# Performance work log

Measured on AMD Instinct MI355X. Metric: run time of the kernel, lower is better.

Reference implementation:

```python
import jax, jax.numpy as jnp
import numpy as np

C = 256  # channels
SHAPES = [(8, C, 80, 80), (8, C, 40, 40), (8, C, 20, 20), (8, C, 10, 10)]
EPS = 1e-8  # torch cosine_similarity eps


def _nearest_resize(x, H, W):
    # Matches F.interpolate(mode='nearest'): src_idx = floor(dst_idx * in/out)
    b, c, h, w = x.shape
    rows = (jnp.arange(H) * h) // H
    cols = (jnp.arange(W) * w) // W
    return x[:, :, rows[:, None], cols[None, :]]


def setup_inputs() -> dict:
    key = jax.random.key(0)
    ks = jax.random.split(key, 12)
    d = {}
    for i, s in enumerate(SHAPES):
        d[f"f{i}"] = jax.random.normal(ks[i], s, dtype=jnp.float32)
        d[f"w{i}"] = jax.random.normal(ks[4 + i], (C, C), dtype=jnp.float32) / jnp.sqrt(jnp.float32(C))
        d[f"b{i}"] = jax.random.normal(ks[8 + i], (C,), dtype=jnp.float32) * 0.01
    return d


def reference(f0, f1, f2, f3, w0, w1, w2, w3, b0, b1, b2, b3):
    feats = [f0, f1, f2, f3]
    ws = [w0, w1, w2, w3]
    bs = [b0, b1, b2, b3]
    H = max(f.shape[2] for f in feats)
    W = max(f.shape[3] for f in feats)
    proj = []
    for f, w, b in zip(feats, ws, bs):
        # 1x1 conv == per-pixel GEMM over channels
        p = jnp.einsum('bchw,oc->bohw', f, w) + b[None, :, None, None]
        if p.shape[2] != H or p.shape[3] != W:
            p = _nearest_resize(p, H, W)
        proj.append(p)
    B = proj[0].shape[0]
    N = len(proj)
    x = jnp.stack(proj, axis=1).reshape(B, N, C, H * W)  # [B,N,C,L]
    # Pairwise cosine similarity along channel dim at each spatial location,
    # then mean over locations (vectorized form of the O(N^2) torch loop).
    dot = jnp.einsum('bicl,bjcl->bijl', x, x)            # [B,N,N,L]
    nrm = jnp.sqrt(jnp.einsum('bicl,bicl->bil', x, x))   # [B,N,L]
    denom = jnp.maximum(nrm[:, :, None, :] * nrm[:, None, :, :], EPS)
    attn = (dot / denom).mean(axis=-1)                   # [B,N,N]
    return jax.nn.softmax(attn, axis=-1)
```

## Files before the change

kernel.cpp:

```cpp
#include <hip/hip_runtime.h>


#define CCH 256
#define WPITCH 40
#define SPITCH 264

typedef __attribute__((ext_vector_type(8))) short short8;
typedef __attribute__((ext_vector_type(4))) short short4_;
typedef __attribute__((ext_vector_type(4))) float float4_;

__device__ inline short f2bf(float x) {
    union { float f; unsigned u; } c; c.f = x;
    unsigned u = c.u + 0x7FFFu + ((c.u >> 16) & 1u);
    return (short)(u >> 16);
}
__device__ inline float bf2f(short b) {
    union { unsigned u; float f; } c; c.u = ((unsigned)(unsigned short)b) << 16;
    return c.f;
}

__device__ inline void dma16(const void* g, void* l) {
    __builtin_amdgcn_global_load_lds(
        (const __attribute__((address_space(1))) void*)g,
        (__attribute__((address_space(3))) void*)l, 16, 0, 0);
}

__global__ __launch_bounds__(256) void proj_small(
    const float* __restrict__ f1, const float* __restrict__ f2,
    const float* __restrict__ f3,
    const float* __restrict__ w0, const float* __restrict__ w1,
    const float* __restrict__ w2, const float* __restrict__ w3,
    const float* __restrict__ b1, const float* __restrict__ b2,
    const float* __restrict__ b3,
    short* __restrict__ u1, short* __restrict__ u2, short* __restrict__ u3,
    short* __restrict__ wp)
{
    __shared__ __align__(16) short Wt[256 * WPITCH];
    __shared__ __align__(16) short Ft[64 * WPITCH];

    const int blk = blockIdx.x;
    const int t = threadIdx.x;

    if (blk >= 272) {
        int id = (blk - 272) * 256 + t;
        int ks = id >> 10;
        int rest = id & 1023;
        int mt = rest >> 6;
        int fl = rest & 63;
        int ln = fl & 15, qd = fl >> 4;
        const float* src = w0 + (size_t)(mt * 16 + ln) * CCH + ks * 32 + qd * 8;
        short8 v;
#pragma unroll
        for (int j = 0; j < 8; ++j) v[j] = f2bf(src[j]);
        *(short8*)(wp + (size_t)id * 8) = v;
        return;
    }

    int b, tile, L;
    const float* F; const float* Wg; const float* bias; short* U;
    if (blk < 200)      { int r = blk;       b = r / 25; tile = r % 25; L = 1600; F = f1; Wg = w1; bias = b1; U = u1; }
    else if (blk < 256) { int r = blk - 200; b = r / 7;  tile = r % 7;  L = 400;  F = f2; Wg = w2; bias = b2; U = u2; }
    else                { int r = blk - 256; b = r / 2;  tile = r % 2;  L = 100;  F = f3; Wg = w3; bias = b3; U = u3; }

    const int lane = t & 63;
    const int wav  = t >> 6;
    const int ln   = lane & 15;
    const int quad = lane >> 4;
    const int pixbase = tile * 64;
    const float* Fb = F + (size_t)b * CCH * L;

    const int wo = t >> 2;
    const int wk = (t & 3) * 8;
    const int fpix = t & 63;
    const int fchunk = t >> 6;
    const int gpix0 = pixbase + fpix;
    const bool pin = gpix0 < L;
    const int gl0 = pin ? gpix0 : 0;

    float4_ wbufA[4], wbufB[4];
    float fbuf[8];
    auto loadW = [&](int ks) {
#pragma unroll
        for (int p = 0; p < 4; ++p) {
            const float* srcp = Wg + (size_t)(p * 64 + wo) * CCH + ks * 32 + wk;
            wbufA[p] = *(const float4_*)srcp;
            wbufB[p] = *(const float4_*)(srcp + 4);
        }
    };
    auto loadF = [&](int ks) {
        const float* fs = Fb + (size_t)(ks * 32 + fchunk * 8) * L + gl0;
#pragma unroll
        for (int j = 0; j < 8; ++j) fbuf[j] = fs[(size_t)j * L];
    };

    float4_ acc[16];
#pragma unroll
    for (int i = 0; i < 16; ++i) acc[i] = (float4_){0.f, 0.f, 0.f, 0.f};

    loadW(0); loadF(0);
    for (int ks = 0; ks < 8; ++ks) {
        __syncthreads();
#pragma unroll
        for (int p = 0; p < 4; ++p) {
            short8 v;
#pragma unroll
            for (int e = 0; e < 4; ++e) { v[e] = f2bf(wbufA[p][e]); v[e + 4] = f2bf(wbufB[p][e]); }
            *(short8*)(&Wt[(p * 64 + wo) * WPITCH + wk]) = v;
        }
        {
            short8 v;
#pragma unroll
            for (int j = 0; j < 8; ++j) v[j] = pin ? f2bf(fbuf[j]) : (short)0;
            *(short8*)(&Ft[fpix * WPITCH + fchunk * 8]) = v;
        }
        __syncthreads();
        const int ksn = (ks + 1) & 7;
        loadW(ksn); loadF(ksn);

        short8 bfrag = *(const short8*)(&Ft[(wav * 16 + ln) * WPITCH + quad * 8]);
#pragma unroll
        for (int mt = 0; mt < 16; ++mt) {
            short8 afrag = *(const short8*)(&Wt[(mt * 16 + ln) * WPITCH + quad * 8]);
            acc[mt] = __builtin_amdgcn_mfma_f32_16x16x32_bf16(afrag, bfrag, acc[mt], 0, 0, 0);
        }
    }

    float ss = 0.f;
#pragma unroll
    for (int mt = 0; mt < 16; ++mt) {
        float4_ bv = *(const float4_*)(bias + mt * 16 + quad * 4);
#pragma unroll
        for (int r = 0; r < 4; ++r) { float v = acc[mt][r] + bv[r]; acc[mt][r] = v; ss += v * v; }
    }
    ss += __shfl_xor(ss, 16);
    ss += __shfl_xor(ss, 32);
    const float inv = 1.f / sqrtf(fmaxf(ss, 1e-24f));

    const int gpixw = pixbase + wav * 16 + ln;
    if (gpixw < L) {
        short* dst = U + ((size_t)b * L + gpixw) * CCH;
#pragma unroll
        for (int mt = 0; mt < 16; ++mt) {
            short4_ v;
#pragma unroll
            for (int r = 0; r < 4; ++r) v[r] = f2bf(acc[mt][r] * inv);
            *(short4_*)(dst + mt * 16 + quad * 4) = v;
        }
    }
}

__global__ __launch_bounds__(256) void proj0_dots(
    const float* __restrict__ F, const short* __restrict__ wp,
    const float* __restrict__ bias,
    const short* __restrict__ u1, const short* __restrict__ u2,
    const short* __restrict__ u3,
    float* __restrict__ partial)
{
    __shared__ __align__(16) char smem[65536];
    short* Wb0 = (short*)smem;
    short* Wb1 = (short*)(smem + 16384);
    float* Fb0 = (float*)(smem + 32768);
    float* Fb1 = (float*)(smem + 49152);
    short* S1 = (short*)smem;
    short* S2 = (short*)(smem + 16896);
    short* S3 = (short*)(smem + 21120);
    float* redF = (float*)(smem + 22176);
    float* redC = (float*)(smem + 22224);

    const int c  = blockIdx.x;
    const int b  = blockIdx.y;
    const int R  = c / 5, C = c - R * 5;
    const int t  = threadIdx.x;
    const int lane = t & 63;
    const int wav  = t >> 6;
    const int ln   = lane & 15;
    const int quad = lane >> 4;
    const float* Fbase = F + (size_t)b * CCH * 6400;

    auto dmaW = [&](int ks, int buf) {
        short* Wb = buf ? Wb1 : Wb0;
#pragma unroll
        for (int m = 0; m < 4; ++m) {
            const int k = wav * 4 + m;
            const short* g = wp + (size_t)ks * 8192 + k * 512 + lane * 8;
            dma16(g, Wb + k * 512);
        }
    };
    auto dmaF = [&](int ks, int buf) {
        float* Fb = buf ? Fb1 : Fb0;
#pragma unroll
        for (int m = 0; m < 4; ++m) {
            const int k = wav * 4 + m;
            const int chl = 2 * k + (lane >> 5);
            const int px4 = (lane & 31) * 4;
            const int gpx = (8 * R + (px4 >> 4)) * 80 + 16 * C + (px4 & 15);
            const float* g = Fbase + (size_t)(ks * 32 + chl) * 6400 + gpx;
            dma16(g, Fb + k * 256);
        }
    };

    float4_ accA[16], accB[16];
#pragma unroll
    for (int i = 0; i < 16; ++i) {
        accA[i] = (float4_){0.f, 0.f, 0.f, 0.f};
        accB[i] = (float4_){0.f, 0.f, 0.f, 0.f};
    }

    const int pxA = wav * 32 + ln;
    const int pxB = pxA + 16;

    dmaW(0, 0); dmaF(0, 0);
    for (int ks = 0; ks < 8; ++ks) {
        __syncthreads();
        if (ks < 7) { dmaW(ks + 1, (ks + 1) & 1); dmaF(ks + 1, (ks + 1) & 1); }
        const short* Wl = (ks & 1) ? Wb1 : Wb0;
        const float* Fl = (ks & 1) ? Fb1 : Fb0;
        short8 bfA, bfB;
#pragma unroll
        for (int j = 0; j < 8; ++j) {
            bfA[j] = f2bf(Fl[(quad * 8 + j) * 128 + pxA]);
            bfB[j] = f2bf(Fl[(quad * 8 + j) * 128 + pxB]);
        }
#pragma unroll
        for (int mt = 0; mt < 16; ++mt) {
            short8 afrag = *(const short8*)(Wl + mt * 512 + lane * 8);
            accA[mt] = __builtin_amdgcn_mfma_f32_16x16x32_bf16(afrag, bfA, accA[mt], 0, 0, 0);
            accB[mt] = __builtin_amdgcn_mfma_f32_16x16x32_bf16(afrag, bfB, accB[mt], 0, 0, 0);
        }
    }

    float ssA = 0.f, ssB = 0.f;
#pragma unroll
    for (int mt = 0; mt < 16; ++mt) {
        float4_ bv = *(const float4_*)(bias + mt * 16 + quad * 4);
#pragma unroll
        for (int r = 0; r < 4; ++r) {
            float vA = accA[mt][r] + bv[r]; accA[mt][r] = vA; ssA += vA * vA;
            float vB = accB[mt][r] + bv[r]; accB[mt][r] = vB; ssB += vB * vB;
        }
    }
    ssA += __shfl_xor(ssA, 16); ssA += __shfl_xor(ssA, 32);
    ssB += __shfl_xor(ssB, 16); ssB += __shfl_xor(ssB, 32);
    const float invA = 1.f / sqrtf(fmaxf(ssA, 1e-24f));
    const float invB = 1.f / sqrtf(fmaxf(ssB, 1e-24f));

    __syncthreads();

    {
        const int p1 = t >> 3, co = (t & 7) * 32;
        const int lr = p1 >> 3, lc = p1 & 7;
        const short* src = u1 + ((size_t)(b * 1600 + (4 * R + lr) * 40 + 8 * C + lc)) * CCH + co;
        short* dst = S1 + p1 * SPITCH + co;
#pragma unroll
        for (int j = 0; j < 4; ++j) *(short8*)(dst + j * 8) = *(const short8*)(src + j * 8);
    }
    if (t < 64) {
        const int p2 = t >> 3, co = (t & 7) * 32;
        const int lr = p2 >> 2, lc = p2 & 3;
        const short* src = u2 + ((size_t)(b * 400 + (2 * R + lr) * 20 + 4 * C + lc)) * CCH + co;
        short* dst = S2 + p2 * SPITCH + co;
#pragma unroll
        for (int j = 0; j < 4; ++j) *(short8*)(dst + j * 8) = *(const short8*)(src + j * 8);
    }
    if (t < 16) {
        const int p3 = t >> 3, co = (t & 7) * 32;
        const short* src = u3 + ((size_t)(b * 100 + R * 10 + 2 * C + p3)) * CCH + co;
        short* dst = S3 + p3 * SPITCH + co;
#pragma unroll
        for (int j = 0; j < 4; ++j) *(short8*)(dst + j * 8) = *(const short8*)(src + j * 8);
    }
    __syncthreads();

    const int c1l = wav * 8 + (ln >> 1);
    const int c2l = (wav >> 1) * 4 + (ln >> 2);
    const int c3l = ln >> 3;
    float d01 = 0.f, d02 = 0.f, d03 = 0.f;
#pragma unroll
    for (int mt = 0; mt < 16; ++mt) {
        const int ch = mt * 16 + quad * 4;
        short4_ v1 = *(const short4_*)(&S1[c1l * SPITCH + ch]);
        short4_ v2 = *(const short4_*)(&S2[c2l * SPITCH + ch]);
        short4_ v3 = *(const short4_*)(&S3[c3l * SPITCH + ch]);
#pragma unroll
        for (int r = 0; r < 4; ++r) {
            float s = accA[mt][r] * invA + accB[mt][r] * invB;
            d01 += s * bf2f(v1[r]);
            d02 += s * bf2f(v2[r]);
            d03 += s * bf2f(v3[r]);
        }
    }
    {
        float vals[3] = {d01, d02, d03};
#pragma unroll
        for (int p = 0; p < 3; ++p) {
            float v = vals[p];
            v += __shfl_xor(v, 1);  v += __shfl_xor(v, 2);  v += __shfl_xor(v, 4);
            v += __shfl_xor(v, 8);  v += __shfl_xor(v, 16); v += __shfl_xor(v, 32);
            if (lane == 0) redF[wav * 3 + p] = v;
        }
    }

    if (wav < 2) {
        const int p1 = wav * 16 + (lane >> 2);
        const int q  = lane & 3;
        const int lr = p1 >> 3, lc = p1 & 7;
        const int par2 = (lr >> 1) * 4 + (lc >> 1);
        const int par3 = lc >> 2;
        float e12 = 0.f, e13 = 0.f;
#pragma unroll
        for (int k = 0; k < 16; ++k) {
            const int co = k * 16 + q * 4;
            short4_ a1 = *(const short4_*)(&S1[p1 * SPITCH + co]);
            short4_ a2 = *(const short4_*)(&S2[par2 * SPITCH + co]);
            short4_ a3 = *(const short4_*)(&S3[par3 * SPITCH + co]);
#pragma unroll
            for (int r = 0; r < 4; ++r) {
                float x1 = bf2f(a1[r]);
                e12 += x1 * bf2f(a2[r]);
                e13 += x1 * bf2f(a3[r]);
            }
        }
        float ev[2] = {e12, e13};
#pragma unroll
        for (int p = 0; p < 2; ++p) {
            float v = ev[p];
            v += __shfl_xor(v, 1);  v += __shfl_xor(v, 2);  v += __shfl_xor(v, 4);
            v += __shfl_xor(v, 8);  v += __shfl_xor(v, 16); v += __shfl_xor(v, 32);
            if (lane == 0) redC[wav * 2 + p] = v;
        }
    } else if (wav == 2) {
        float e23 = 0.f;
        if (lane < 32) {
            const int p2 = lane >> 2;
            const int q  = lane & 3;
            const int par3 = (p2 & 3) >> 1;
#pragma unroll
            for (int k = 0; k < 16; ++k) {
                const int co = k * 16 + q * 4;
                short4_ a2 = *(const short4_*)(&S2[p2 * SPITCH + co]);
                short4_ a3 = *(const short4_*)(&S3[par3 * SPITCH + co]);
#pragma unroll
                for (int r = 0; r < 4; ++r) e23 += bf2f(a2[r]) * bf2f(a3[r]);
            }
        }
        e23 += __shfl_xor(e23, 1);  e23 += __shfl_xor(e23, 2);  e23 += __shfl_xor(e23, 4);
        e23 += __shfl_xor(e23, 8);  e23 += __shfl_xor(e23, 16); e23 += __shfl_xor(e23, 32);
        if (lane == 0) redC[4] = e23;
    }
    __syncthreads();

    if (t < 6) {
        float v;
        if (t < 3) {
            v = 0.f;
#pragma unroll
            for (int w = 0; w < 4; ++w) v += redF[w * 3 + t];
        } else if (t == 3) v = redC[0] + redC[2];
        else if (t == 4)   v = redC[1] + redC[3];
        else               v = redC[4];
        partial[((size_t)b * 6 + t) * 50 + c] = v;
    }
}

__global__ void softmax4(const float* __restrict__ partial, float* __restrict__ out) {
    int t = threadIdx.x;
    if (t >= 128) return;
    int b = t >> 4, i = (t >> 2) & 3, j = t & 3;
    float a[4];
#pragma unroll
    for (int jj = 0; jj < 4; ++jj) {
        if (jj == i) { a[jj] = 1.0f; continue; }
        int lo = i < jj ? i : jj;
        int hi = i < jj ? jj : i;
        int pidx;
        if (lo == 0) pidx = hi - 1;
        else if (lo == 1) pidx = 1 + hi;
        else pidx = 5;
        const float* pp = partial + ((size_t)b * 6 + pidx) * 50;
        float s = 0.f;
        for (int k = 0; k < 50; ++k) s += pp[k];
        int rf = 80 >> lo;
        a[jj] = s / (float)(rf * rf);
    }
    float m = fmaxf(fmaxf(a[0], a[1]), fmaxf(a[2], a[3]));
    float e0 = expf(a[0] - m), e1 = expf(a[1] - m), e2 = expf(a[2] - m), e3 = expf(a[3] - m);
    float sum = e0 + e1 + e2 + e3;
    float ev = (j == 0) ? e0 : (j == 1) ? e1 : (j == 2) ? e2 : e3;
    out[t] = ev / sum;
}

extern "C" void kernel_launch(void* const* d_in, const int* in_sizes, int n_in,
                              void* d_out, int out_size, void* d_ws, size_t ws_size,
                              hipStream_t stream) {
    const float* f[4]  = {(const float*)d_in[0], (const float*)d_in[3],
                          (const float*)d_in[6], (const float*)d_in[9]};
    const float* w[4]  = {(const float*)d_in[1], (const float*)d_in[4],
                          (const float*)d_in[7], (const float*)d_in[10]};
    const float* bs[4] = {(const float*)d_in[2], (const float*)d_in[5],
                          (const float*)d_in[8], (const float*)d_in[11]};

    char* ws = (char*)d_ws;
    size_t off = 0;
    short* u1 = (short*)(ws + off); off += (size_t)8 * CCH * 1600 * sizeof(short);
    short* u2 = (short*)(ws + off); off += (size_t)8 * CCH * 400  * sizeof(short);
    short* u3 = (short*)(ws + off); off += (size_t)8 * CCH * 100  * sizeof(short);
    short* wp = (short*)(ws + off); off += (size_t)65536 * sizeof(short);
    float* partial = (float*)(ws + off);

    proj_small<<<304, 256, 0, stream>>>(f[1], f[2], f[3],
                                        w[0], w[1], w[2], w[3],
                                        bs[1], bs[2], bs[3],
                                        u1, u2, u3, wp);

    proj0_dots<<<dim3(50, 8), 256, 0, stream>>>(f[0], wp, bs[0],
                                                u1, u2, u3, partial);

    softmax4<<<1, 128, 0, stream>>>(partial, (float*)d_out);
}
```

Before: 155.7 us.

## Double tile size per block with 512 threads and deeper prefetch pipeline

The fused level-0 projection and dot kernel now covers a 16x16 pixel tile with 512 threads and 98KB of dynamic LDS, so the grid shrinks from 400 to 200 blocks. The K loop prefetches two stages ahead and uses explicit vmcnt waits and raw barriers in place of a full __syncthreads, so global-to-LDS DMA overlaps MFMA work. Each block loads the weight slice once for twice as many pixels, which halves redundant weight traffic. The cost is fewer blocks on a 256-CU device, lower occupancy from the large LDS use, and fragile hand-written waitcnt counts.

```diff
diff --git a/kernel.cpp b/kernel.cpp
--- a/kernel.cpp
+++ b/kernel.cpp
@@ -149,23 +149,23 @@
     }
 }
 
-__global__ __launch_bounds__(256) void proj0_dots(
+__global__ __launch_bounds__(512, 2) void proj0_dots(
     const float* __restrict__ F, const short* __restrict__ wp,
     const float* __restrict__ bias,
     const short* __restrict__ u1, const short* __restrict__ u2,
     const short* __restrict__ u3,
     float* __restrict__ partial)
 {
-    __shared__ __align__(16) char smem[65536];
+    extern __shared__ __align__(16) char smem[];
     short* Wb0 = (short*)smem;
     short* Wb1 = (short*)(smem + 16384);
     float* Fb0 = (float*)(smem + 32768);
-    float* Fb1 = (float*)(smem + 49152);
+    float* Fb1 = (float*)(smem + 65536);
     short* S1 = (short*)smem;
-    short* S2 = (short*)(smem + 16896);
-    short* S3 = (short*)(smem + 21120);
-    float* redF = (float*)(smem + 22176);
-    float* redC = (float*)(smem + 22224);
+    short* S2 = (short*)(smem + 33792);
+    short* S3 = (short*)(smem + 42240);
+    float* redF = (float*)(smem + 44352);
+    float* redC = (float*)(smem + 44448);
 
     const int c  = blockIdx.x;
     const int b  = blockIdx.y;
@@ -180,22 +180,18 @@
     auto dmaW = [&](int ks, int buf) {
         short* Wb = buf ? Wb1 : Wb0;
 #pragma unroll
-        for (int m = 0; m < 4; ++m) {
-            const int k = wav * 4 + m;
-            const short* g = wp + (size_t)ks * 8192 + k * 512 + lane * 8;
-            dma16(g, Wb + k * 512);
+        for (int m = 0; m < 2; ++m) {
+            const int k = wav * 2 + m;
+            dma16(wp + (size_t)ks * 8192 + k * 512 + lane * 8, Wb + k * 512);
         }
     };
     auto dmaF = [&](int ks, int buf) {
         float* Fb = buf ? Fb1 : Fb0;
+        const int gpx = (16 * R + (lane >> 2)) * 80 + 16 * C + (lane & 3) * 4;
 #pragma unroll
         for (int m = 0; m < 4; ++m) {
             const int k = wav * 4 + m;
-            const int chl = 2 * k + (lane >> 5);
-            const int px4 = (lane & 31) * 4;
-            const int gpx = (8 * R + (px4 >> 4)) * 80 + 16 * C + (px4 & 15);
-            const float* g = Fbase + (size_t)(ks * 32 + chl) * 6400 + gpx;
-            dma16(g, Fb + k * 256);
+            dma16(Fbase + (size_t)(ks * 32 + k) * 6400 + gpx, Fb + k * 256);
         }
     };
 
@@ -210,16 +206,20 @@
     const int pxB = pxA + 16;
 
     dmaW(0, 0); dmaF(0, 0);
+    dmaW(1, 1); dmaF(1, 1);
+#pragma unroll
     for (int ks = 0; ks < 8; ++ks) {
-        __syncthreads();
-        if (ks < 7) { dmaW(ks + 1, (ks + 1) & 1); dmaF(ks + 1, (ks + 1) & 1); }
+        if (ks < 7) asm volatile("s_waitcnt vmcnt(6)" ::: "memory");
+        else        asm volatile("s_waitcnt vmcnt(0)" ::: "memory");
+        __builtin_amdgcn_s_barrier();
+
         const short* Wl = (ks & 1) ? Wb1 : Wb0;
         const float* Fl = (ks & 1) ? Fb1 : Fb0;
         short8 bfA, bfB;
 #pragma unroll
         for (int j = 0; j < 8; ++j) {
-            bfA[j] = f2bf(Fl[(quad * 8 + j) * 128 + pxA]);
-            bfB[j] = f2bf(Fl[(quad * 8 + j) * 128 + pxB]);
+            bfA[j] = f2bf(Fl[(quad * 8 + j) * 256 + pxA]);
+            bfB[j] = f2bf(Fl[(quad * 8 + j) * 256 + pxB]);
         }
 #pragma unroll
         for (int mt = 0; mt < 16; ++mt) {
@@ -227,6 +227,12 @@
             accA[mt] = __builtin_amdgcn_mfma_f32_16x16x32_bf16(afrag, bfA, accA[mt], 0, 0, 0);
             accB[mt] = __builtin_amdgcn_mfma_f32_16x16x32_bf16(afrag, bfB, accB[mt], 0, 0, 0);
         }
+
+        if (ks < 6) {
+            asm volatile("s_waitcnt lgkmcnt(0)" ::: "memory");
+            __builtin_amdgcn_s_barrier();
+            dmaW(ks + 2, ks & 1); dmaF(ks + 2, ks & 1);
+        }
     }
 
     float ssA = 0.f, ssB = 0.f;
@@ -249,22 +255,23 @@
     {
         const int p1 = t >> 3, co = (t & 7) * 32;
         const int lr = p1 >> 3, lc = p1 & 7;
-        const short* src = u1 + ((size_t)(b * 1600 + (4 * R + lr) * 40 + 8 * C + lc)) * CCH + co;
+        const short* src = u1 + ((size_t)(b * 1600 + (8 * R + lr) * 40 + 8 * C + lc)) * CCH + co;
         short* dst = S1 + p1 * SPITCH + co;
 #pragma unroll
         for (int j = 0; j < 4; ++j) *(short8*)(dst + j * 8) = *(const short8*)(src + j * 8);
     }
-    if (t < 64) {
+    if (t < 128) {
         const int p2 = t >> 3, co = (t & 7) * 32;
         const int lr = p2 >> 2, lc = p2 & 3;
-        const short* src = u2 + ((size_t)(b * 400 + (2 * R + lr) * 20 + 4 * C + lc)) * CCH + co;
+        const short* src = u2 + ((size_t)(b * 400 + (4 * R + lr) * 20 + 4 * C + lc)) * CCH + co;
         short* dst = S2 + p2 * SPITCH + co;
 #pragma unroll
         for (int j = 0; j < 4; ++j) *(short8*)(dst + j * 8) = *(const short8*)(src + j * 8);
     }
-    if (t < 16) {
+    if (t < 32) {
         const int p3 = t >> 3, co = (t & 7) * 32;
-        const short* src = u3 + ((size_t)(b * 100 + R * 10 + 2 * C + p3)) * CCH + co;
+        const int lr = p3 >> 1, lc = p3 & 1;
+        const short* src = u3 + ((size_t)(b * 100 + (2 * R + lr) * 10 + 2 * C + lc)) * CCH + co;
         short* dst = S3 + p3 * SPITCH + co;
 #pragma unroll
         for (int j = 0; j < 4; ++j) *(short8*)(dst + j * 8) = *(const short8*)(src + j * 8);
@@ -273,7 +280,7 @@
 
     const int c1l = wav * 8 + (ln >> 1);
     const int c2l = (wav >> 1) * 4 + (ln >> 2);
-    const int c3l = ln >> 3;
+    const int c3l = (wav >> 2) * 2 + (ln >> 3);
     float d01 = 0.f, d02 = 0.f, d03 = 0.f;
 #pragma unroll
     for (int mt = 0; mt < 16; ++mt) {
@@ -300,12 +307,12 @@
         }
     }
 
-    if (wav < 2) {
+    if (wav < 4) {
         const int p1 = wav * 16 + (lane >> 2);
         const int q  = lane & 3;
         const int lr = p1 >> 3, lc = p1 & 7;
         const int par2 = (lr >> 1) * 4 + (lc >> 1);
-        const int par3 = lc >> 2;
+        const int par3 = (lr >> 2) * 2 + (lc >> 2);
         float e12 = 0.f, e13 = 0.f;
 #pragma unroll
         for (int k = 0; k < 16; ++k) {
@@ -328,24 +335,23 @@
             v += __shfl_xor(v, 8);  v += __shfl_xor(v, 16); v += __shfl_xor(v, 32);
             if (lane == 0) redC[wav * 2 + p] = v;
         }
-    } else if (wav == 2) {
+    } else if (wav == 4) {
+        const int p2 = lane >> 2;
+        const int q  = lane & 3;
+        const int lr = p2 >> 2, lc = p2 & 3;
+        const int par3 = (lr >> 1) * 2 + (lc >> 1);
         float e23 = 0.f;
-        if (lane < 32) {
-            const int p2 = lane >> 2;
-            const int q  = lane & 3;
-            const int par3 = (p2 & 3) >> 1;
-#pragma unroll
-            for (int k = 0; k < 16; ++k) {
-                const int co = k * 16 + q * 4;
-                short4_ a2 = *(const short4_*)(&S2[p2 * SPITCH + co]);
-                short4_ a3 = *(const short4_*)(&S3[par3 * SPITCH + co]);
-#pragma unroll
-                for (int r = 0; r < 4; ++r) e23 += bf2f(a2[r]) * bf2f(a3[r]);
-            }
+#pragma unroll
+        for (int k = 0; k < 16; ++k) {
+            const int co = k * 16 + q * 4;
+            short4_ a2 = *(const short4_*)(&S2[p2 * SPITCH + co]);
+            short4_ a3 = *(const short4_*)(&S3[par3 * SPITCH + co]);
+#pragma unroll
+            for (int r = 0; r < 4; ++r) e23 += bf2f(a2[r]) * bf2f(a3[r]);
         }
         e23 += __shfl_xor(e23, 1);  e23 += __shfl_xor(e23, 2);  e23 += __shfl_xor(e23, 4);
         e23 += __shfl_xor(e23, 8);  e23 += __shfl_xor(e23, 16); e23 += __shfl_xor(e23, 32);
-        if (lane == 0) redC[4] = e23;
+        if (lane == 0) redC[8] = e23;
     }
     __syncthreads();
 
@@ -354,11 +360,11 @@
         if (t < 3) {
             v = 0.f;
 #pragma unroll
-            for (int w = 0; w < 4; ++w) v += redF[w * 3 + t];
-        } else if (t == 3) v = redC[0] + redC[2];
-        else if (t == 4)   v = redC[1] + redC[3];
-        else               v = redC[4];
-        partial[((size_t)b * 6 + t) * 50 + c] = v;
+            for (int w = 0; w < 8; ++w) v += redF[w * 3 + t];
+        } else if (t == 3) v = redC[0] + redC[2] + redC[4] + redC[6];
+        else if (t == 4)   v = redC[1] + redC[3] + redC[5] + redC[7];
+        else               v = redC[8];
+        partial[((size_t)b * 6 + t) * 25 + c] = v;
     }
 }
 
@@ -376,9 +382,9 @@
         if (lo == 0) pidx = hi - 1;
         else if (lo == 1) pidx = 1 + hi;
         else pidx = 5;
-        const float* pp = partial + ((size_t)b * 6 + pidx) * 50;
+        const float* pp = partial + ((size_t)b * 6 + pidx) * 25;
         float s = 0.f;
-        for (int k = 0; k < 50; ++k) s += pp[k];
+        for (int k = 0; k < 25; ++k) s += pp[k];
         int rf = 80 >> lo;
         a[jj] = s / (float)(rf * rf);
     }
@@ -407,13 +413,20 @@
     short* wp = (short*)(ws + off); off += (size_t)65536 * sizeof(short);
     float* partial = (float*)(ws + off);
 
+    static int smax_set = 0;
+    if (!smax_set) {
+        hipFuncSetAttribute(reinterpret_cast<const void*>(proj0_dots),
+                            hipFuncAttributeMaxDynamicSharedMemorySize, 98304);
+        smax_set = 1;
+    }
+
     proj_small<<<304, 256, 0, stream>>>(f[1], f[2], f[3],
                                         w[0], w[1], w[2], w[3],
                                         bs[1], bs[2], bs[3],
                                         u1, u2, u3, wp);
 
-    proj0_dots<<<dim3(50, 8), 256, 0, stream>>>(f[0], wp, bs[0],
-                                                u1, u2, u3, partial);
+    proj0_dots<<<dim3(25, 8), 512, 98304, stream>>>(f[0], wp, bs[0],
+                                                    u1, u2, u3, partial);
 
     softmax4<<<1, 128, 0, stream>>>(partial, (float*)d_out);
 }
```

Measured after the change: 145.9 us. 6.3% less time.
